# Kernel optimization log

Measured on AMD Instinct MI355X. Metric: run time of the kernel, lower is better.

The kernel has to match this reference:

```python
import jax, jax.numpy as jnp
import numpy as np

N = 100000
EPS = 1e-5


def setup_inputs() -> dict:
    key = jax.random.key(0)
    ks = jax.random.split(key, 12)
    x = jax.random.normal(ks[0], (N, 128), dtype=jnp.float32)
    edge_index = jax.random.randint(ks[1], (2, 1600000), 0, N, dtype=jnp.int64)
    def lin(k, fi, fo):
        s = 1.0 / np.sqrt(fi)
        return jax.random.uniform(k, (fi, fo), jnp.float32, -s, s)
    return {
        "x": x, "edge_index": edge_index,
        "W0": lin(ks[2], 128, 128), "b0": jnp.zeros((128,), jnp.float32),
        "g0": jnp.ones((128,), jnp.float32), "be0": jnp.zeros((128,), jnp.float32),
        "W1": lin(ks[3], 128, 128), "b1": jnp.zeros((128,), jnp.float32),
        "g1": jnp.ones((128,), jnp.float32), "be1": jnp.zeros((128,), jnp.float32),
        "W2": lin(ks[4], 128, 40), "b2": jnp.zeros((40,), jnp.float32),
    }


def _gcn_norm(edge_index):
    # add self-loops, symmetric normalization deg^-1/2 A deg^-1/2
    loops = jnp.arange(N, dtype=edge_index.dtype)
    src = jnp.concatenate([edge_index[0], loops])
    dst = jnp.concatenate([edge_index[1], loops])
    deg = jax.ops.segment_sum(jnp.ones_like(dst, dtype=jnp.float32), dst, num_segments=N)
    dinv = jnp.where(deg > 0, jax.lax.rsqrt(deg), 0.0)
    norm = dinv[src] * dinv[dst]
    return src, dst, norm


def _conv(x, W, b, src, dst, norm):
    xw = x @ W  # [N, F_out]
    agg = jax.ops.segment_sum(norm[:, None] * xw[src], dst, num_segments=N)
    return agg + b


def _bn(x, g, b):
    mu = jnp.mean(x, axis=0)
    var = jnp.var(x, axis=0)
    return (x - mu) * jax.lax.rsqrt(var + EPS) * g + b


def reference(x, edge_index, W0, b0, g0, be0, W1, b1, g1, be1, W2, b2):
    src, dst, norm = _gcn_norm(edge_index)
    h = _conv(x, W0, b0, src, dst, norm)
    h = jax.nn.relu(_bn(h, g0, be0))
    h = _conv(h, W1, b1, src, dst, norm)
    h = jax.nn.relu(_bn(h, g1, be1))
    h = _conv(h, W2, b2, src, dst, norm)
    return jax.nn.log_softmax(h, axis=-1)
```

## Files before the change

kernel.cpp:

```cpp
#include <hip/hip_runtime.h>
#include <math.h>

#define NN 100000
#define NE 1600000
#define EPSF 1e-5f
#define NB 391
#define BKN 256
#define CAP 4864
#define CHA 4096

typedef unsigned short u16;
typedef unsigned int u32;
typedef __attribute__((ext_vector_type(8))) short bf16x8;
typedef __attribute__((ext_vector_type(4))) float f32x4;
typedef __attribute__((ext_vector_type(8))) unsigned short u16x8;

__device__ __forceinline__ u16 f2bf(float f) {
    u32 u = __float_as_uint(f);
    u32 r = (u + 0x7fffu + ((u >> 16) & 1u)) >> 16;
    return (u16)r;
}
__device__ __forceinline__ float bf_lo(u32 u) { return __uint_as_float(u << 16); }
__device__ __forceinline__ float bf_hi(u32 u) { return __uint_as_float(u & 0xffff0000u); }

__global__ void k_zero_ints(int* p, int n) {
    int i = blockIdx.x * 256 + threadIdx.x;
    if (i < n) p[i] = 0;
}

__global__ __launch_bounds__(256) void k_prept(const float* __restrict__ W0,
                                               const float* __restrict__ W1,
                                               const float* __restrict__ W2,
                                               u16* __restrict__ wt0,
                                               u16* __restrict__ wt1,
                                               u16* __restrict__ wt2) {
    int b = blockIdx.x, t = threadIdx.x;
    if (b < 8) {
        for (int idx = t; idx < 16 * 128; idx += 256) {
            int k = b * 16 + (idx >> 7), c = idx & 127;
            wt0[c * 128 + k] = f2bf(W0[k * 128 + c]);
        }
    } else if (b < 16) {
        for (int idx = t; idx < 16 * 128; idx += 256) {
            int k = (b - 8) * 16 + (idx >> 7), c = idx & 127;
            wt1[c * 128 + k] = f2bf(W1[k * 128 + c]);
        }
    } else {
        for (int idx = t; idx < 16 * 64; idx += 256) {
            int k = (b - 16) * 16 + (idx >> 6), c = idx & 63;
            wt2[c * 128 + k] = f2bf(c < 40 ? W2[k * 40 + c] : 0.f);
        }
    }
}

__global__ __launch_bounds__(256) void k_bscatter(const int* __restrict__ src,
                                                  const int* __restrict__ dst,
                                                  int* __restrict__ gcur,
                                                  u32* __restrict__ bkt) {
    __shared__ int hist[NB];
    __shared__ int base[NB];
    int t = threadIdx.x;
    long e0 = (long)blockIdx.x * CHA;
    for (int i = t; i < NB; i += 256) hist[i] = 0;
    __syncthreads();
#pragma unroll
    for (int i = 0; i < CHA / 256; i++) {
        long e = e0 + i * 256 + t;
        if (e < NE) atomicAdd(&hist[dst[e] >> 8], 1);
    }
    __syncthreads();
    for (int i = t; i < NB; i += 256)
        base[i] = i * CAP + atomicAdd(&gcur[i], hist[i]);
    __syncthreads();
    for (int i = t; i < NB; i += 256) hist[i] = 0;
    __syncthreads();
#pragma unroll
    for (int i = 0; i < CHA / 256; i++) {
        long e = e0 + i * 256 + t;
        if (e < NE) {
            int d = dst[e];
            int s = src[e];
            int b = d >> 8;
            int r = atomicAdd(&hist[b], 1);
            bkt[base[b] + r] = (u32)s | ((u32)(d & 255) << 17);
        }
    }
}

__global__ __launch_bounds__(BKN) void k_csr(const u32* __restrict__ bkt,
                                             const int* __restrict__ gcur,
                                             u32* __restrict__ rsd,
                                             int* __restrict__ csr,
                                             float* __restrict__ dinv) {
    __shared__ int cnt[BKN];
    __shared__ int tmp[BKN];
    __shared__ int cur[BKN];
    int t = threadIdx.x, b = blockIdx.x;
    int ebase = b * CAP;
    int m = gcur[b];
    cnt[t] = 0;
    __syncthreads();
    for (int i = t; i < m; i += BKN)
        atomicAdd(&cnt[(bkt[ebase + i] >> 17) & 255], 1);
    __syncthreads();
    int v = cnt[t];
    tmp[t] = v;
    __syncthreads();
    for (int o = 1; o < BKN; o <<= 1) {
        int u = (t >= o) ? tmp[t - o] : 0;
        __syncthreads();
        tmp[t] += u;
        __syncthreads();
    }
    int excl = tmp[t] - v;
    int node = b * BKN + t;
    if (node < NN) {
        rsd[node] = ((u32)(ebase + excl) << 8) | (u32)v;
        dinv[node] = rsqrtf((float)(v + 1));
    }
    cur[t] = ebase + excl;
    __syncthreads();
    for (int i = t; i < m; i += BKN) {
        u32 p = bkt[ebase + i];
        int pos = atomicAdd(&cur[(p >> 17) & 255], 1);
        csr[pos] = (int)(p & 0x1FFFFu);
    }
}

__global__ __launch_bounds__(256) void k_gemm128m_f0(const float* __restrict__ X,
                                                     const u16* __restrict__ WtG,
                                                     u16* __restrict__ Y, int n) {
    __shared__ u16 Xl[128][136];
    __shared__ u16 Wt[128][136];
    int t = threadIdx.x;
    int row0 = blockIdx.x * 128;

#pragma unroll
    for (int i = 0; i < 16; i++) {
        int idx = t + i * 256;
        int r = idx >> 5, q = idx & 31;
        int gr = row0 + r;
        float4 v = make_float4(0.f, 0.f, 0.f, 0.f);
        if (gr < n) v = reinterpret_cast<const float4*>(X + (size_t)gr * 128)[q];
        ushort4 o;
        o.x = f2bf(v.x); o.y = f2bf(v.y); o.z = f2bf(v.z); o.w = f2bf(v.w);
        *reinterpret_cast<ushort4*>(&Xl[r][q * 4]) = o;
    }
#pragma unroll
    for (int i = 0; i < 8; i++) {
        int idx = t + i * 256;
        int r = idx >> 4, q = idx & 15;
        *reinterpret_cast<u16x8*>(&Wt[r][q * 8]) =
            *reinterpret_cast<const u16x8*>(&WtG[r * 128 + q * 8]);
    }
    __syncthreads();

    int lane = t & 63, w = t >> 6;
    int wr = (w >> 1) * 64, wc = (w & 1) * 64;
    int fr = lane & 15;
    int fs = (lane >> 4) * 8;
    f32x4 acc[4][4] = {};
#pragma unroll
    for (int ks = 0; ks < 4; ks++) {
        bf16x8 a[4], b[4];
#pragma unroll
        for (int m = 0; m < 4; m++)
            a[m] = *reinterpret_cast<const bf16x8*>(&Xl[wr + m * 16 + fr][ks * 32 + fs]);
#pragma unroll
        for (int c = 0; c < 4; c++)
            b[c] = *reinterpret_cast<const bf16x8*>(&Wt[wc + c * 16 + fr][ks * 32 + fs]);
#pragma unroll
        for (int m = 0; m < 4; m++)
#pragma unroll
            for (int c = 0; c < 4; c++)
                acc[m][c] = __builtin_amdgcn_mfma_f32_16x16x32_bf16(a[m], b[c], acc[m][c], 0, 0, 0);
    }

    int crow = (lane >> 4) * 4, ccol = lane & 15;
#pragma unroll
    for (int m = 0; m < 4; m++) {
#pragma unroll
        for (int c = 0; c < 4; c++) {
#pragma unroll
            for (int rg = 0; rg < 4; rg++) {
                int grow = row0 + wr + m * 16 + crow + rg;
                if (grow < n)
                    Y[(size_t)grow * 128 + wc + c * 16 + ccol] = f2bf(acc[m][c][rg]);
            }
        }
    }
}

__global__ __launch_bounds__(256) void k_gemm128m_b1(const u32* __restrict__ Xb,
                                                     const u16* __restrict__ WtG,
                                                     u16* __restrict__ Y, int n,
                                                     const float* __restrict__ stats,
                                                     const float* __restrict__ g,
                                                     const float* __restrict__ be) {
    __shared__ u16 Xl[128][136];
    __shared__ u16 Wt[128][136];
    __shared__ float ssc[128], ssh[128];
    int t = threadIdx.x;
    int row0 = blockIdx.x * 128;

    if (t < 128) {
        float mu = stats[t] * (1.0f / NN);
        float var = stats[128 + t] * (1.0f / NN) - mu * mu;
        float sc = rsqrtf(var + EPSF) * g[t];
        ssc[t] = sc;
        ssh[t] = be[t] - mu * sc;
    }
    __syncthreads();

#pragma unroll
    for (int i = 0; i < 8; i++) {
        int idx = t + i * 256;
        int r = idx >> 4, q = idx & 15;
        int gr = row0 + r;
        uint4 vv = make_uint4(0u, 0u, 0u, 0u);
        if (gr < n) vv = reinterpret_cast<const uint4*>(Xb + (size_t)gr * 64)[q];
        float f[8] = { bf_lo(vv.x), bf_hi(vv.x), bf_lo(vv.y), bf_hi(vv.y),
                       bf_lo(vv.z), bf_hi(vv.z), bf_lo(vv.w), bf_hi(vv.w) };
        u16x8 o;
#pragma unroll
        for (int e = 0; e < 8; e++) {
            int fi = q * 8 + e;
            float x = fmaxf(fmaf(f[e], ssc[fi], ssh[fi]), 0.f);
            o[e] = f2bf(x);
        }
        *reinterpret_cast<u16x8*>(&Xl[r][q * 8]) = o;
    }
#pragma unroll
    for (int i = 0; i < 8; i++) {
        int idx = t + i * 256;
        int r = idx >> 4, q = idx & 15;
        *reinterpret_cast<u16x8*>(&Wt[r][q * 8]) =
            *reinterpret_cast<const u16x8*>(&WtG[r * 128 + q * 8]);
    }
    __syncthreads();

    int lane = t & 63, w = t >> 6;
    int wr = (w >> 1) * 64, wc = (w & 1) * 64;
    int fr = lane & 15;
    int fs = (lane >> 4) * 8;
    f32x4 acc[4][4] = {};
#pragma unroll
    for (int ks = 0; ks < 4; ks++) {
        bf16x8 a[4], b[4];
#pragma unroll
        for (int m = 0; m < 4; m++)
            a[m] = *reinterpret_cast<const bf16x8*>(&Xl[wr + m * 16 + fr][ks * 32 + fs]);
#pragma unroll
        for (int c = 0; c < 4; c++)
            b[c] = *reinterpret_cast<const bf16x8*>(&Wt[wc + c * 16 + fr][ks * 32 + fs]);
#pragma unroll
        for (int m = 0; m < 4; m++)
#pragma unroll
            for (int c = 0; c < 4; c++)
                acc[m][c] = __builtin_amdgcn_mfma_f32_16x16x32_bf16(a[m], b[c], acc[m][c], 0, 0, 0);
    }

    int crow = (lane >> 4) * 4, ccol = lane & 15;
#pragma unroll
    for (int m = 0; m < 4; m++) {
#pragma unroll
        for (int c = 0; c < 4; c++) {
#pragma unroll
            for (int rg = 0; rg < 4; rg++) {
                int grow = row0 + wr + m * 16 + crow + rg;
                if (grow < n)
                    Y[(size_t)grow * 128 + wc + c * 16 + ccol] = f2bf(acc[m][c][rg]);
            }
        }
    }
}

__global__ __launch_bounds__(256) void k_gemm40m(const u32* __restrict__ Xb,
                                                 const u16* __restrict__ WtG,
                                                 u16* __restrict__ Y, int n,
                                                 const float* __restrict__ stats,
                                                 const float* __restrict__ g,
                                                 const float* __restrict__ be) {
    __shared__ u16 Xl[128][136];
    __shared__ u16 Wt[64][136];
    __shared__ float ssc[128], ssh[128];
    int t = threadIdx.x;
    int row0 = blockIdx.x * 128;

    if (t < 128) {
        float mu = stats[t] * (1.0f / NN);
        float var = stats[128 + t] * (1.0f / NN) - mu * mu;
        float sc = rsqrtf(var + EPSF) * g[t];
        ssc[t] = sc;
        ssh[t] = be[t] - mu * sc;
    }
    __syncthreads();

#pragma unroll
    for (int i = 0; i < 8; i++) {
        int idx = t + i * 256;
        int r = idx >> 4, q = idx & 15;
        int gr = row0 + r;
        uint4 vv = make_uint4(0u, 0u, 0u, 0u);
        if (gr < n) vv = reinterpret_cast<const uint4*>(Xb + (size_t)gr * 64)[q];
        float f[8] = { bf_lo(vv.x), bf_hi(vv.x), bf_lo(vv.y), bf_hi(vv.y),
                       bf_lo(vv.z), bf_hi(vv.z), bf_lo(vv.w), bf_hi(vv.w) };
        u16x8 o;
#pragma unroll
        for (int e = 0; e < 8; e++) {
            int fi = q * 8 + e;
            float x = fmaxf(fmaf(f[e], ssc[fi], ssh[fi]), 0.f);
            o[e] = f2bf(x);
        }
        *reinterpret_cast<u16x8*>(&Xl[r][q * 8]) = o;
    }
#pragma unroll
    for (int i = 0; i < 4; i++) {
        int idx = t + i * 256;
        int r = idx >> 4, q = idx & 15;
        *reinterpret_cast<u16x8*>(&Wt[r][q * 8]) =
            *reinterpret_cast<const u16x8*>(&WtG[r * 128 + q * 8]);
    }
    __syncthreads();

    int lane = t & 63, w = t >> 6;
    int wr = w * 32;
    int fr = lane & 15;
    int fs = (lane >> 4) * 8;
    f32x4 acc[2][4] = {};
#pragma unroll
    for (int ks = 0; ks < 4; ks++) {
        bf16x8 a[2], b[4];
#pragma unroll
        for (int m = 0; m < 2; m++)
            a[m] = *reinterpret_cast<const bf16x8*>(&Xl[wr + m * 16 + fr][ks * 32 + fs]);
#pragma unroll
        for (int c = 0; c < 4; c++)
            b[c] = *reinterpret_cast<const bf16x8*>(&Wt[c * 16 + fr][ks * 32 + fs]);
#pragma unroll
        for (int m = 0; m < 2; m++)
#pragma unroll
            for (int c = 0; c < 4; c++)
                acc[m][c] = __builtin_amdgcn_mfma_f32_16x16x32_bf16(a[m], b[c], acc[m][c], 0, 0, 0);
    }

    int crow = (lane >> 4) * 4, ccol = lane & 15;
#pragma unroll
    for (int m = 0; m < 2; m++) {
#pragma unroll
        for (int c = 0; c < 3; c++) {
#pragma unroll
            for (int rg = 0; rg < 4; rg++) {
                int grow = row0 + wr + m * 16 + crow + rg;
                int gcol = c * 16 + ccol;
                if (grow < n && gcol < 40)
                    Y[(size_t)grow * 64 + gcol] = f2bf(acc[m][c][rg]);
            }
        }
    }
}

__global__ __launch_bounds__(256) void k_gather128s(const u32* __restrict__ xwb,
                                                    u32* __restrict__ aggb,
                                                    const u32* __restrict__ rsd,
                                                    const int* __restrict__ csr,
                                                    const float* __restrict__ dinv,
                                                    float* __restrict__ stats) {
    __shared__ float red[1024];
    int t = threadIdx.x;
    int w = t >> 6, l = t & 63;
    int nb = blockIdx.x * 32 + w * 8;
    float sx = 0.f, sy = 0.f, sxx = 0.f, syy = 0.f;
    for (int i = 0; i < 8; i++) {
        int node = nb + i;
        if (node >= NN) break;
        float dd = dinv[node];
        u32 us = xwb[(size_t)node * 64 + l];
        float ax = dd * dd * bf_lo(us);
        float ay = dd * dd * bf_hi(us);
        u32 rs = rsd[node];
        int p = (int)(rs >> 8);
        int pe = p + (int)(rs & 255u);
        while (p < pe) {
            int cnt = pe - p;
            if (cnt > 64) cnt = 64;
            int myidx = 0;
            float mydv = 0.f;
            if (l < cnt) {
                myidx = csr[p + l];
                mydv  = dd * dinv[myidx];
            }
            int j = 0;
            for (; j + 4 <= cnt; j += 4) {
                int s0 = __shfl(myidx, j);
                int s1 = __shfl(myidx, j + 1);
                int s2 = __shfl(myidx, j + 2);
                int s3 = __shfl(myidx, j + 3);
                float c0 = __shfl(mydv, j);
                float c1 = __shfl(mydv, j + 1);
                float c2 = __shfl(mydv, j + 2);
                float c3 = __shfl(mydv, j + 3);
                u32 u0 = xwb[(size_t)s0 * 64 + l];
                u32 u1 = xwb[(size_t)s1 * 64 + l];
                u32 u2 = xwb[(size_t)s2 * 64 + l];
                u32 u3 = xwb[(size_t)s3 * 64 + l];
                ax += c0 * bf_lo(u0) + c1 * bf_lo(u1) + c2 * bf_lo(u2) + c3 * bf_lo(u3);
                ay += c0 * bf_hi(u0) + c1 * bf_hi(u1) + c2 * bf_hi(u2) + c3 * bf_hi(u3);
            }
            for (; j < cnt; j++) {
                int s = __shfl(myidx, j);
                float c = __shfl(mydv, j);
                u32 u = xwb[(size_t)s * 64 + l];
                ax += c * bf_lo(u);
                ay += c * bf_hi(u);
            }
            p += cnt;
        }
        aggb[(size_t)node * 64 + l] = (u32)f2bf(ax) | ((u32)f2bf(ay) << 16);
        sx += ax; sxx += ax * ax;
        sy += ay; syy += ay * ay;
    }
    red[w * 128 + 2 * l]     = sx;
    red[w * 128 + 2 * l + 1] = sy;
    red[512 + w * 128 + 2 * l]     = sxx;
    red[512 + w * 128 + 2 * l + 1] = syy;
    __syncthreads();
    if (t < 128) {
        float s  = red[t] + red[128 + t] + red[256 + t] + red[384 + t];
        float s2 = red[512 + t] + red[640 + t] + red[768 + t] + red[896 + t];
        atomicAdd(&stats[t], s);
        atomicAdd(&stats[128 + t], s2);
    }
}

__global__ __launch_bounds__(256) void k_gather40_lsm(const u16* __restrict__ xwb,
                                                      const float* __restrict__ b2,
                                                      float* __restrict__ out,
                                                      const u32* __restrict__ rsd,
                                                      const int* __restrict__ csr,
                                                      const float* __restrict__ dinv) {
    int node = blockIdx.x * 4 + (threadIdx.x >> 6);
    if (node >= NN) return;
    int lane = threadIdx.x & 63;
    float dd = dinv[node];
    float acc = 0.f;
    if (lane < 40) acc = dd * dd * __uint_as_float((u32)xwb[(size_t)node * 64 + lane] << 16);
    u32 rs = rsd[node];
    int p = (int)(rs >> 8);
    int pe = p + (int)(rs & 255u);
    while (p < pe) {
        int cnt = pe - p;
        if (cnt > 64) cnt = 64;
        int myidx = 0;
        float mydv = 0.f;
        if (lane < cnt) {
            myidx = csr[p + lane];
            mydv  = dd * dinv[myidx];
        }
        int j = 0;
        for (; j + 2 <= cnt; j += 2) {
            int sA = __shfl(myidx, j);
            int sB = __shfl(myidx, j + 1);
            float cA = __shfl(mydv, j);
            float cB = __shfl(mydv, j + 1);
            float vA = 0.f, vB = 0.f;
            if (lane < 40) {
                vA = __uint_as_float((u32)xwb[(size_t)sA * 64 + lane] << 16);
                vB = __uint_as_float((u32)xwb[(size_t)sB * 64 + lane] << 16);
            }
            acc += cA * vA + cB * vB;
        }
        if (j < cnt) {
            int s = __shfl(myidx, j);
            float c = __shfl(mydv, j);
            if (lane < 40) acc += c * __uint_as_float((u32)xwb[(size_t)s * 64 + lane] << 16);
        }
        p += cnt;
    }
    float v = (lane < 40) ? acc + b2[lane] : -1e30f;
    float m = v;
#pragma unroll
    for (int o = 32; o; o >>= 1) m = fmaxf(m, __shfl_xor(m, o));
    float ex = (lane < 40) ? expf(v - m) : 0.f;
    float sum = ex;
#pragma unroll
    for (int o = 32; o; o >>= 1) sum += __shfl_xor(sum, o);
    if (lane < 40) out[(size_t)node * 40 + lane] = v - m - logf(sum);
}

extern "C" void kernel_launch(void* const* d_in, const int* in_sizes, int n_in,
                              void* d_out, int out_size, void* d_ws, size_t ws_size,
                              hipStream_t stream) {
    const float* x  = (const float*)d_in[0];
    const int* ei   = (const int*)d_in[1];
    const int* src  = ei;
    const int* dst  = ei + NE;
    const float* W0 = (const float*)d_in[2];
    const float* g0 = (const float*)d_in[4];
    const float* be0= (const float*)d_in[5];
    const float* W1 = (const float*)d_in[6];
    const float* g1 = (const float*)d_in[8];
    const float* be1= (const float*)d_in[9];
    const float* W2 = (const float*)d_in[10];
    const float* b2 = (const float*)d_in[11];
    float* out = (float*)d_out;

    float* ws      = (float*)d_ws;
    float* dinv    = ws;
    float* stats0  = ws + 100000;
    float* stats1  = ws + 100256;
    int* gcur      = (int*)(ws + 100512);
    u32* rsd       = (u32*)(ws + 100912);
    u16* wt0       = (u16*)(ws + 200912);
    u16* wt1       = (u16*)(ws + 209104);
    u16* wt2       = (u16*)(ws + 217296);
    u32* bkt       = (u32*)(ws + 221392);
    int* csr       = (int*)(ws + 2123216);
    u16* bufA16    = (u16*)(ws + 4025040);
    u32* bufB      = (u32*)(ws + 10425040);

    k_zero_ints<<<4, 256, 0, stream>>>((int*)stats0, 903);
    k_prept<<<24, 256, 0, stream>>>(W0, W1, W2, wt0, wt1, wt2);
    k_bscatter<<<(NE + CHA - 1) / CHA, 256, 0, stream>>>(src, dst, gcur, bkt);
    k_csr<<<NB, BKN, 0, stream>>>(bkt, gcur, rsd, csr, dinv);

    int gm = (NN + 127) / 128;
    int gs = (NN + 31) / 32;

    k_gemm128m_f0<<<gm, 256, 0, stream>>>(x, wt0, bufA16, NN);
    k_gather128s<<<gs, 256, 0, stream>>>((const u32*)bufA16, bufB, rsd, csr, dinv, stats0);

    k_gemm128m_b1<<<gm, 256, 0, stream>>>(bufB, wt1, bufA16, NN, stats0, g0, be0);
    k_gather128s<<<gs, 256, 0, stream>>>((const u32*)bufA16, bufB, rsd, csr, dinv, stats1);

    k_gemm40m<<<gm, 256, 0, stream>>>(bufB, wt2, bufA16, NN, stats1, g1, be1);
    k_gather40_lsm<<<(NN + 3) / 4, 256, 0, stream>>>(bufA16, b2, out, rsd, csr, dinv);
}
```

Measured before the change: 468.7 us.

## Split 128-wide gather into feature halves pinned to XCD groups for L2 locality

The 128-feature gather kernel is split so each block handles only 64 of the 128 features (one half of each row). Block IDs are remapped so that blocks on XCDs 0-3 handle the first half and XCDs 4-7 the second, which shrinks each XCD's gathered working set and is meant to raise L2 hit rates. Each wavefront now processes two nodes at once, one per 32-lane half. The cost is twice as many blocks, half-width 128-byte row reads, extra CSR and dinv reads, and divergence when the two nodes in a wave have different degrees. The code assumes the round-robin block-to-XCD dispatch order.

```diff
diff --git a/kernel.cpp b/kernel.cpp
--- a/kernel.cpp
+++ b/kernel.cpp
@@ -360,76 +360,95 @@
     }
 }
 
-__global__ __launch_bounds__(256) void k_gather128s(const u32* __restrict__ xwb,
+__global__ __launch_bounds__(256) void k_gather128h(const u32* __restrict__ xwb,
                                                     u32* __restrict__ aggb,
                                                     const u32* __restrict__ rsd,
                                                     const int* __restrict__ csr,
                                                     const float* __restrict__ dinv,
                                                     float* __restrict__ stats) {
-    __shared__ float red[1024];
+    __shared__ float red[256];
+    __shared__ float red2[256];
     int t = threadIdx.x;
     int w = t >> 6, l = t & 63;
-    int nb = blockIdx.x * 32 + w * 8;
+    int lc = l & 31;
+    int sub = l >> 5;
+    int bid = blockIdx.x;
+    int xcd = bid & 7;
+    int half = xcd >> 2;
+    int grp = (bid >> 3) * 4 + (xcd & 3);
+    if (grp >= (NN + 31) / 32) return;
+    int fbase = half * 32;
+
     float sx = 0.f, sy = 0.f, sxx = 0.f, syy = 0.f;
-    for (int i = 0; i < 8; i++) {
-        int node = nb + i;
-        if (node >= NN) break;
+    for (int it = 0; it < 4; it++) {
+        int node = grp * 32 + w * 8 + it * 2 + sub;
         float dd = dinv[node];
-        u32 us = xwb[(size_t)node * 64 + l];
+        u32 us = xwb[(size_t)node * 64 + fbase + lc];
         float ax = dd * dd * bf_lo(us);
         float ay = dd * dd * bf_hi(us);
         u32 rs = rsd[node];
         int p = (int)(rs >> 8);
         int pe = p + (int)(rs & 255u);
-        while (p < pe) {
-            int cnt = pe - p;
-            if (cnt > 64) cnt = 64;
+        int sbase = l & 32;
+        while (true) {
+            int rem = pe - p;
+            int cnt = rem > 32 ? 32 : (rem > 0 ? rem : 0);
+            if (!__any(cnt > 0)) break;
             int myidx = 0;
             float mydv = 0.f;
-            if (l < cnt) {
-                myidx = csr[p + l];
+            if (lc < cnt) {
+                myidx = csr[p + lc];
                 mydv  = dd * dinv[myidx];
             }
+            int cmax = cnt;
+            int co = __shfl(cnt, l ^ 32);
+            if (co > cmax) cmax = co;
             int j = 0;
-            for (; j + 4 <= cnt; j += 4) {
-                int s0 = __shfl(myidx, j);
-                int s1 = __shfl(myidx, j + 1);
-                int s2 = __shfl(myidx, j + 2);
-                int s3 = __shfl(myidx, j + 3);
-                float c0 = __shfl(mydv, j);
-                float c1 = __shfl(mydv, j + 1);
-                float c2 = __shfl(mydv, j + 2);
-                float c3 = __shfl(mydv, j + 3);
-                u32 u0 = xwb[(size_t)s0 * 64 + l];
-                u32 u1 = xwb[(size_t)s1 * 64 + l];
-                u32 u2 = xwb[(size_t)s2 * 64 + l];
-                u32 u3 = xwb[(size_t)s3 * 64 + l];
+            for (; j + 4 <= cmax; j += 4) {
+                int s0 = __shfl(myidx, sbase + j);
+                int s1 = __shfl(myidx, sbase + j + 1);
+                int s2 = __shfl(myidx, sbase + j + 2);
+                int s3 = __shfl(myidx, sbase + j + 3);
+                float c0 = __shfl(mydv, sbase + j);
+                float c1 = __shfl(mydv, sbase + j + 1);
+                float c2 = __shfl(mydv, sbase + j + 2);
+                float c3 = __shfl(mydv, sbase + j + 3);
+                u32 u0 = xwb[(size_t)s0 * 64 + fbase + lc];
+                u32 u1 = xwb[(size_t)s1 * 64 + fbase + lc];
+                u32 u2 = xwb[(size_t)s2 * 64 + fbase + lc];
+                u32 u3 = xwb[(size_t)s3 * 64 + fbase + lc];
                 ax += c0 * bf_lo(u0) + c1 * bf_lo(u1) + c2 * bf_lo(u2) + c3 * bf_lo(u3);
                 ay += c0 * bf_hi(u0) + c1 * bf_hi(u1) + c2 * bf_hi(u2) + c3 * bf_hi(u3);
             }
-            for (; j < cnt; j++) {
-                int s = __shfl(myidx, j);
-                float c = __shfl(mydv, j);
-                u32 u = xwb[(size_t)s * 64 + l];
+            for (; j < cmax; j++) {
+                int s = __shfl(myidx, sbase + j);
+                float c = __shfl(mydv, sbase + j);
+                u32 u = xwb[(size_t)s * 64 + fbase + lc];
                 ax += c * bf_lo(u);
                 ay += c * bf_hi(u);
             }
             p += cnt;
         }
-        aggb[(size_t)node * 64 + l] = (u32)f2bf(ax) | ((u32)f2bf(ay) << 16);
+        aggb[(size_t)node * 64 + fbase + lc] = (u32)f2bf(ax) | ((u32)f2bf(ay) << 16);
         sx += ax; sxx += ax * ax;
         sy += ay; syy += ay * ay;
     }
-    red[w * 128 + 2 * l]     = sx;
-    red[w * 128 + 2 * l + 1] = sy;
-    red[512 + w * 128 + 2 * l]     = sxx;
-    red[512 + w * 128 + 2 * l + 1] = syy;
-    __syncthreads();
-    if (t < 128) {
-        float s  = red[t] + red[128 + t] + red[256 + t] + red[384 + t];
-        float s2 = red[512 + t] + red[640 + t] + red[768 + t] + red[896 + t];
-        atomicAdd(&stats[t], s);
-        atomicAdd(&stats[128 + t], s2);
+    sx  += __shfl_xor(sx, 32);
+    sy  += __shfl_xor(sy, 32);
+    sxx += __shfl_xor(sxx, 32);
+    syy += __shfl_xor(syy, 32);
+    if (l < 32) {
+        red[w * 64 + lc * 2]      = sx;
+        red[w * 64 + lc * 2 + 1]  = sy;
+        red2[w * 64 + lc * 2]     = sxx;
+        red2[w * 64 + lc * 2 + 1] = syy;
+    }
+    __syncthreads();
+    if (t < 64) {
+        float s  = red[t] + red[64 + t] + red[128 + t] + red[192 + t];
+        float s2 = red2[t] + red2[64 + t] + red2[128 + t] + red2[192 + t];
+        atomicAdd(&stats[half * 64 + t], s);
+        atomicAdd(&stats[128 + half * 64 + t], s2);
     }
 }
 
@@ -525,13 +544,13 @@
     k_csr<<<NB, BKN, 0, stream>>>(bkt, gcur, rsd, csr, dinv);
 
     int gm = (NN + 127) / 128;
-    int gs = (NN + 31) / 32;
+    int gh = 782 * 8;
 
     k_gemm128m_f0<<<gm, 256, 0, stream>>>(x, wt0, bufA16, NN);
-    k_gather128s<<<gs, 256, 0, stream>>>((const u32*)bufA16, bufB, rsd, csr, dinv, stats0);
+    k_gather128h<<<gh, 256, 0, stream>>>((const u32*)bufA16, bufB, rsd, csr, dinv, stats0);
 
     k_gemm128m_b1<<<gm, 256, 0, stream>>>(bufB, wt1, bufA16, NN, stats0, g0, be0);
-    k_gather128s<<<gs, 256, 0, stream>>>((const u32*)bufA16, bufB, rsd, csr, dinv, stats1);
+    k_gather128h<<<gh, 256, 0, stream>>>((const u32*)bufA16, bufB, rsd, csr, dinv, stats1);
 
     k_gemm40m<<<gm, 256, 0, stream>>>(bufB, wt2, bufA16, NN, stats1, g1, be1);
     k_gather40_lsm<<<(NN + 3) / 4, 256, 0, stream>>>(bufA16, b2, out, rsd, csr, dinv);
```

Result: slower. 478.8 us (+2.1%).
